# Kernel tuning notes

Measured on AMD Instinct MI355X. Metric: run time of the kernel, lower is better.

## Reference

```python
import jax, jax.numpy as jnp
import numpy as np

B, T, D, H, O, E = 4, 2048, 1024, 2048, 1024, 8
EPS = 1e-12  # torch F.normalize p=1 eps


def setup_inputs() -> dict:
    key = jax.random.key(0)
    ks = jax.random.split(key, 8)
    s = lambda *dims: 1.0 / np.sqrt(dims[0])
    return {
        "x": jax.random.normal(ks[0], (B, T, D), dtype=jnp.float32),
        "num_experts_chosen": 2,
        "W_gate": jax.random.normal(ks[1], (D, E), dtype=jnp.float32) * s(D),
        "b_gate": jnp.zeros((E,), dtype=jnp.float32),
        "W1": jax.random.normal(ks[2], (E, D, H), dtype=jnp.float32) * s(D),
        "b1": jnp.zeros((E, H), dtype=jnp.float32),
        "W2": jax.random.normal(ks[3], (E, H, O), dtype=jnp.float32) * s(H),
        "b2": jnp.zeros((E, O), dtype=jnp.float32),
    }


def reference(x, num_experts_chosen, W_gate, b_gate, W1, b1, W2, b2):
    # Router: softmax over experts -> [b, t, E]
    gating = jax.nn.softmax(jnp.einsum("btd,de->bte", x, W_gate) + b_gate, axis=-1)

    # Top-k mask (scatter of ones at top-k indices), then L1 renormalize
    _, topk_idx = jax.lax.top_k(gating, num_experts_chosen)  # [b, t, k]
    mask = jax.nn.one_hot(topk_idx, E, dtype=gating.dtype).sum(axis=-2)  # [b, t, E]
    g = gating * mask
    g = g / jnp.maximum(jnp.sum(jnp.abs(g), axis=-1, keepdims=True), EPS)

    # Dense compute of ALL experts (faithful to original), eval-mode dropout = identity
    h = jax.nn.relu(jnp.einsum("btd,edh->bteh", x, W1) + b1)  # [b, t, E, H]
    eo = jnp.einsum("bteh,eho->bteo", h, W2) + b2              # [b, t, E, O]

    # Weighted combine over experts
    return jnp.einsum("bte,bteo->bto", g, eo)
```

## Files before the change

kernel.cpp:

```cpp
#include <hip/hip_runtime.h>
#include <hip/hip_bf16.h>

typedef unsigned short u16;
typedef __attribute__((ext_vector_type(8))) short short8;
typedef __attribute__((ext_vector_type(4))) float floatx4;

#define NB 4
#define NT 2048
#define ND 1024
#define NH 2048
#define NO 1024
#define NE 8
#define NTOK (NB * NT)

#define BM2 256
#define BN2 256
#define BKT 64
#define TBUF 16384

__device__ __forceinline__ u16 f2bf(float f) {
  __hip_bfloat16 h = __float2bfloat16(f);
  return *reinterpret_cast<u16*>(&h);
}

__device__ __forceinline__ float bf2f(unsigned u) {
  return __uint_as_float(u << 16);
}

__device__ __forceinline__ void async16(const u16* g, u16* l) {
  __builtin_amdgcn_global_load_lds(
      (const __attribute__((address_space(1))) void*)g,
      (__attribute__((address_space(3))) void*)l, 16, 0, 0);
}

__global__ __launch_bounds__(256) void transpose_cvt(
    const float* __restrict__ in, u16* __restrict__ out, int R, int C) {
  __shared__ float tile[64][65];
  int e = blockIdx.z;
  in  += (size_t)e * R * C;
  out += (size_t)e * R * C;
  int c0 = blockIdx.x * 64, r0 = blockIdx.y * 64;
  int t = threadIdx.x;
#pragma unroll
  for (int i = 0; i < 4; ++i) {
    int idx = t + i * 256;
    int r = idx >> 4, cq = idx & 15;
    float4 v = *(const float4*)&in[(size_t)(r0 + r) * C + c0 + cq * 4];
    tile[r][cq * 4 + 0] = v.x; tile[r][cq * 4 + 1] = v.y;
    tile[r][cq * 4 + 2] = v.z; tile[r][cq * 4 + 3] = v.w;
  }
  __syncthreads();
#pragma unroll
  for (int i = 0; i < 4; ++i) {
    int idx = t + i * 256;
    int c = idx >> 4, rq = idx & 15;
    uint2 p;
    p.x = (unsigned)f2bf(tile[rq * 4 + 0][c]) | ((unsigned)f2bf(tile[rq * 4 + 1][c]) << 16);
    p.y = (unsigned)f2bf(tile[rq * 4 + 2][c]) | ((unsigned)f2bf(tile[rq * 4 + 3][c]) << 16);
    *(uint2*)&out[(size_t)(c0 + c) * R + r0 + rq * 4] = p;
  }
}

__global__ __launch_bounds__(256) void router_kernel(
    const float* __restrict__ x, const float* __restrict__ Wg,
    const float* __restrict__ bg, u16* __restrict__ xbf,
    int* __restrict__ counts, int* __restrict__ entries,
    float* __restrict__ wts) {
  __shared__ int   se0[32], se1[32];
  __shared__ float sw0[32], sw1[32];
  int t = threadIdx.x;
  int tl = t >> 3;
  int l8 = t & 7;
  int tok = blockIdx.x * 32 + tl;

  const float* xrow = x + (size_t)tok * ND;
  u16* xbrow = xbf + (size_t)tok * ND;
  float acc[8] = {};
#pragma unroll 4
  for (int i = 0; i < 32; ++i) {
    int d0 = l8 * 4 + i * 32;
    float4 xv = *(const float4*)&xrow[d0];
    uint2 p;
    p.x = (unsigned)f2bf(xv.x) | ((unsigned)f2bf(xv.y) << 16);
    p.y = (unsigned)f2bf(xv.z) | ((unsigned)f2bf(xv.w) << 16);
    *(uint2*)&xbrow[d0] = p;
    const float* wr = Wg + (size_t)d0 * NE;
#pragma unroll
    for (int j = 0; j < 4; ++j) {
      float xs = (j == 0) ? xv.x : (j == 1) ? xv.y : (j == 2) ? xv.z : xv.w;
      float4 w0 = *(const float4*)&wr[j * NE];
      float4 w1 = *(const float4*)&wr[j * NE + 4];
      acc[0] += xs * w0.x; acc[1] += xs * w0.y;
      acc[2] += xs * w0.z; acc[3] += xs * w0.w;
      acc[4] += xs * w1.x; acc[5] += xs * w1.y;
      acc[6] += xs * w1.z; acc[7] += xs * w1.w;
    }
  }
#pragma unroll
  for (int off = 4; off; off >>= 1)
#pragma unroll
    for (int k = 0; k < 8; ++k) acc[k] += __shfl_down(acc[k], off, 8);

  if (l8 == 0) {
    float best = -1e30f, second = -1e30f;
    int e0 = 0, e1 = 0;
#pragma unroll
    for (int i = 0; i < NE; ++i) {
      float L = acc[i] + bg[i];
      if (L > best) { second = best; e1 = e0; best = L; e0 = i; }
      else if (L > second) { second = L; e1 = i; }
    }
    float p1 = __expf(second - best);
    float inv = 1.f / (1.f + p1);
    se0[tl] = e0; se1[tl] = e1;
    sw0[tl] = inv; sw1[tl] = p1 * inv;
  }
  __syncthreads();

  if (t < NE) {
    int e = t;
    int c = 0;
#pragma unroll
    for (int k = 0; k < 32; ++k) c += (se0[k] == e) + (se1[k] == e);
    int pos = atomicAdd(&counts[e * 32], c);
    int base = blockIdx.x * 32;
    for (int k = 0; k < 32; ++k) {
      if (se0[k] == e) { entries[e * NTOK + pos] = (base + k) * 2;     wts[e * NTOK + pos] = sw0[k]; ++pos; }
      if (se1[k] == e) { entries[e * NTOK + pos] = (base + k) * 2 + 1; wts[e * NTOK + pos] = sw1[k]; ++pos; }
    }
  }
}

template<int KD, int NTILES, bool G2>
__global__ __launch_bounds__(512, 2) void gemm_moe(
    const u16* __restrict__ A, const u16* __restrict__ Bw,
    const float* __restrict__ bias, const int* __restrict__ counts,
    const int* __restrict__ entries, const float* __restrict__ wts,
    u16* __restrict__ out) {
  constexpr int LDO = NTILES * 256;
  constexpr int NI  = KD / 128;

  int b = blockIdx.x;
  int e = b & 7;
  int r = b >> 3;
  int m0 = (r / NTILES) * BM2;
  int n0 = (r % NTILES) * BN2;
  int cnt = counts[e * 32];
  if (m0 >= cnt) return;
  int rem = cnt - m0; if (rem > BM2) rem = BM2;

  __shared__ __align__(16) u16 As[2 * TBUF];
  __shared__ __align__(16) u16 Bs[2 * TBUF];
  __shared__ int   ent_s[BM2];
  __shared__ float w_s[BM2];

  int t = threadIdx.x;
  if (t < BM2) {
    int src = (t < rem) ? (e * NTOK + m0 + t) : (e * NTOK);
    ent_s[t] = entries[src];
    if constexpr (G2) w_s[t] = wts[src];
  }
  __syncthreads();

  int lane = t & 63, wv = t >> 6;
  int wr = wv >> 2, wc = wv & 3;

  int srow = lane >> 3;
  int sc   = ((lane & 7) ^ (srow & 7)) * 8;
  const u16* aS[2][2];
  const u16* bS[2][2];
#pragma unroll
  for (int h = 0; h < 2; ++h)
#pragma unroll
    for (int d = 0; d < 2; ++d) {
      int rowl = h * 128 + wv * 16 + d * 8 + srow;
      int ent = ent_s[rowl];
      size_t ra = G2 ? (size_t)ent : (size_t)(ent >> 1);
      aS[h][d] = A + ra * KD + sc;
      bS[h][d] = Bw + (size_t)e * LDO * KD + (size_t)(n0 + rowl) * KD + sc;
    }

#define STAGE_A(buf, half, ko) do { int _k = (ko); if (_k >= KD) _k = 0;    \
    async16(aS[half][0] + _k, As + (buf)*TBUF + (half)*8192 + wv*1024);      \
    async16(aS[half][1] + _k, As + (buf)*TBUF + (half)*8192 + wv*1024 + 512);\
  } while (0)
#define STAGE_B(buf, half, ko) do { int _k = (ko); if (_k >= KD) _k = 0;    \
    async16(bS[half][0] + _k, Bs + (buf)*TBUF + (half)*8192 + wv*1024);      \
    async16(bS[half][1] + _k, Bs + (buf)*TBUF + (half)*8192 + wv*1024 + 512);\
  } while (0)

  int rA = lane & 15, q = lane >> 4;
  int aRow = (wr * 64 + rA) * 64;
  int bRow = (wc * 32 + rA) * 64;
  int ch0 = ((q) ^ (rA & 7)) * 8;
  int ch1 = ((4 + q) ^ (rA & 7)) * 8;

  short8 a[2][4];
  short8 bb[2][2][2];
  floatx4 acc[2][2][4][2] = {};

#define LDA(mh, buf) do {                                                   \
    const u16* _p = As + (buf)*TBUF + (mh)*8192 + aRow;                      \
    _Pragma("unroll") for (int f = 0; f < 4; ++f) {                          \
      a[0][f] = *(const short8*)(_p + f*1024 + ch0);                         \
      a[1][f] = *(const short8*)(_p + f*1024 + ch1); } } while (0)
#define LDB(nh, buf) do {                                                   \
    const u16* _p = Bs + (buf)*TBUF + (nh)*8192 + bRow;                      \
    _Pragma("unroll") for (int nf = 0; nf < 2; ++nf) {                       \
      bb[nh][0][nf] = *(const short8*)(_p + nf*1024 + ch0);                  \
      bb[nh][1][nf] = *(const short8*)(_p + nf*1024 + ch1); } } while (0)
#define MM(mh, nh)                                                           \
    __builtin_amdgcn_s_setprio(1);                                           \
    _Pragma("unroll") for (int kk = 0; kk < 2; ++kk)                         \
    _Pragma("unroll") for (int f = 0; f < 4; ++f)                            \
    _Pragma("unroll") for (int nf = 0; nf < 2; ++nf)                         \
      acc[mh][nh][f][nf] = __builtin_amdgcn_mfma_f32_16x16x32_bf16(          \
          a[kk][f], bb[nh][kk][nf], acc[mh][nh][f][nf], 0, 0, 0);            \
    __builtin_amdgcn_s_setprio(0);
#define SCH __builtin_amdgcn_sched_barrier(0)
#define BAR __builtin_amdgcn_s_barrier()
#define LGK asm volatile("s_waitcnt lgkmcnt(0)")
#define VM6 asm volatile("s_waitcnt vmcnt(6)")

  STAGE_A(0, 0, 0);  STAGE_B(0, 0, 0);  STAGE_A(0, 1, 0);  STAGE_B(0, 1, 0);
  STAGE_A(1, 0, 64); STAGE_B(1, 0, 64); STAGE_A(1, 1, 64);
  SCH; VM6; SCH; BAR;

  for (int it = 0; it < NI; ++it) {
    int kb = it * 128;
    LDA(0, 0); LDB(0, 0);
    STAGE_B(1, 1, 64 + kb);
    SCH; BAR; LGK; SCH;
    MM(0, 0);
    SCH; BAR;
    LDB(1, 0);
    STAGE_A(0, 0, 128 + kb);
    SCH; BAR; LGK; SCH;
    MM(0, 1);
    SCH; BAR;
    LDA(1, 0);
    STAGE_B(0, 0, 128 + kb);
    SCH; BAR; LGK; SCH;
    MM(1, 0);
    SCH; BAR;
    STAGE_A(0, 1, 128 + kb);
    SCH; BAR; LGK; SCH;
    MM(1, 1);
    SCH; VM6; SCH; BAR;
    LDA(0, 1); LDB(0, 1);
    STAGE_B(0, 1, 128 + kb);
    SCH; BAR; LGK; SCH;
    MM(0, 0);
    SCH; BAR;
    LDB(1, 1);
    STAGE_A(1, 0, 192 + kb);
    SCH; BAR; LGK; SCH;
    MM(0, 1);
    SCH; BAR;
    LDA(1, 1);
    STAGE_B(1, 0, 192 + kb);
    SCH; BAR; LGK; SCH;
    MM(1, 0);
    SCH; BAR;
    STAGE_A(1, 1, 192 + kb);
    SCH; BAR; LGK; SCH;
    MM(1, 1);
    SCH; VM6; SCH; BAR;
  }
  SCH;
  asm volatile("s_waitcnt vmcnt(0)");
  SCH;

  float bcol[2][2];
#pragma unroll
  for (int nh = 0; nh < 2; ++nh)
#pragma unroll
    for (int nf = 0; nf < 2; ++nf)
      bcol[nh][nf] = bias[e * LDO + n0 + wc * 32 + nh * 128 + nf * 16 + rA];

#pragma unroll
  for (int mh = 0; mh < 2; ++mh)
#pragma unroll
    for (int f = 0; f < 4; ++f)
#pragma unroll
      for (int rr = 0; rr < 4; ++rr) {
        int lm = wr * 64 + mh * 128 + f * 16 + q * 4 + rr;
        if (lm >= rem) continue;
        int ent = ent_s[lm];
        float wgt = 1.f;
        if constexpr (G2) wgt = w_s[lm];
        u16* dst = out + (size_t)ent * LDO + n0;
#pragma unroll
        for (int nh = 0; nh < 2; ++nh)
#pragma unroll
          for (int nf = 0; nf < 2; ++nf) {
            int col = wc * 32 + nh * 128 + nf * 16 + rA;
            float v = acc[mh][nh][f][nf][rr] + bcol[nh][nf];
            if constexpr (G2) v *= wgt; else v = fmaxf(v, 0.f);
            dst[col] = f2bf(v);
          }
      }
#undef STAGE_A
#undef STAGE_B
#undef LDA
#undef LDB
#undef MM
#undef SCH
#undef BAR
#undef LGK
#undef VM6
}

__global__ __launch_bounds__(256) void combine_kernel(
    const u16* __restrict__ eo, float* __restrict__ out) {
  size_t idx = (size_t)blockIdx.x * 256 + threadIdx.x;
  size_t tok = idx >> 8;
  int oq = (int)(idx & 255) * 4;
  const u16* p0 = eo + (tok * 2) * NO + oq;
  const u16* p1 = p0 + NO;
  uint2 ua = *(const uint2*)p0;
  uint2 ub = *(const uint2*)p1;
  float4 o;
  o.x = bf2f(ua.x & 0xffff) + bf2f(ub.x & 0xffff);
  o.y = bf2f(ua.x >> 16)    + bf2f(ub.x >> 16);
  o.z = bf2f(ua.y & 0xffff) + bf2f(ub.y & 0xffff);
  o.w = bf2f(ua.y >> 16)    + bf2f(ub.y >> 16);
  *(float4*)&out[tok * NO + oq] = o;
}

extern "C" void kernel_launch(void* const* d_in, const int* in_sizes, int n_in,
                              void* d_out, int out_size, void* d_ws, size_t ws_size,
                              hipStream_t stream) {
  (void)in_sizes; (void)n_in; (void)out_size; (void)ws_size;
  const float* x  = (const float*)d_in[0];
  const float* Wg = (const float*)d_in[2];
  const float* bg = (const float*)d_in[3];
  const float* W1 = (const float*)d_in[4];
  const float* b1 = (const float*)d_in[5];
  const float* W2 = (const float*)d_in[6];
  const float* b2 = (const float*)d_in[7];
  float* out = (float*)d_out;

  char* ws = (char*)d_ws;
  size_t off = 0;
  int*   counts  = (int*)(ws + off);   off += NE * 32 * 4;
  int*   entries = (int*)(ws + off);   off += (size_t)NE * NTOK * 4;
  float* wts     = (float*)(ws + off); off += (size_t)NE * NTOK * 4;
  u16*   xbf     = (u16*)(ws + off);   off += (size_t)NTOK * ND * 2;
  u16*   w1t     = (u16*)(ws + off);   off += (size_t)NE * NH * ND * 2;
  u16*   w2t     = (u16*)(ws + off);   off += (size_t)NE * NO * NH * 2;
  u16*   hbuf    = (u16*)(ws + off);   off += (size_t)NTOK * 2 * NH * 2;
  u16*   eo      = w1t;

  hipMemsetAsync(counts, 0, NE * 32 * 4, stream);

  transpose_cvt<<<dim3(NH / 64, ND / 64, NE), 256, 0, stream>>>(W1, w1t, ND, NH);
  transpose_cvt<<<dim3(NO / 64, NH / 64, NE), 256, 0, stream>>>(W2, w2t, NH, NO);
  router_kernel<<<NTOK / 32, 256, 0, stream>>>(x, Wg, bg, xbf, counts, entries, wts);
  gemm_moe<ND, 8, false><<<NE * (NTOK / BM2) * 8, 512, 0, stream>>>(
      xbf, w1t, b1, counts, entries, wts, hbuf);
  gemm_moe<NH, 4, true ><<<NE * (NTOK / BM2) * 4, 512, 0, stream>>>(
      hbuf, w2t, b2, counts, entries, wts, eo);
  combine_kernel<<<(NTOK * NO / 4) / 256, 256, 0, stream>>>(eo, out);
}
```

Measured before the change: 482.8 us.

## Add triple-buffered async-LDS gather GEMM for first expert layer

Adds a new gemm_flow kernel that uses a three-stage LDS ring with BK=32 slices, issuing global_load_lds for tile k+2 while running MFMAs on tile k, with one barrier per iteration, a vmcnt wait, and raised wave priority around the MFMA block. It replaces gemm_moe for the first (x·W1, ReLU) GEMM only. The goal is to hide global-load latency behind compute with a simpler steady-state pipeline. In exchange it uses 96 KB of LDS per block, which may limit occupancy, and it takes more loop iterations with smaller K slices.

```diff
diff --git a/kernel.cpp b/kernel.cpp
--- a/kernel.cpp
+++ b/kernel.cpp
@@ -15,7 +15,6 @@
 
 #define BM2 256
 #define BN2 256
-#define BKT 64
 #define TBUF 16384
 
 __device__ __forceinline__ u16 f2bf(float f) {
@@ -127,6 +126,125 @@
     for (int k = 0; k < 32; ++k) {
       if (se0[k] == e) { entries[e * NTOK + pos] = (base + k) * 2;     wts[e * NTOK + pos] = sw0[k]; ++pos; }
       if (se1[k] == e) { entries[e * NTOK + pos] = (base + k) * 2 + 1; wts[e * NTOK + pos] = sw1[k]; ++pos; }
+    }
+  }
+}
+
+template<int KD, int NTILES, bool G2>
+__global__ __launch_bounds__(512, 2) void gemm_flow(
+    const u16* __restrict__ A, const u16* __restrict__ Bw,
+    const float* __restrict__ bias, const int* __restrict__ counts,
+    const int* __restrict__ entries, const float* __restrict__ wts,
+    u16* __restrict__ out) {
+  constexpr int LDO = NTILES * 256;
+  constexpr int NKT = KD / 32;
+
+  int b = blockIdx.x;
+  int e = b & 7;
+  int r = b >> 3;
+  int m0 = (r / NTILES) * BM2;
+  int n0 = (r % NTILES) * BN2;
+  int cnt = counts[e * 32];
+  if (m0 >= cnt) return;
+  int rem = cnt - m0; if (rem > BM2) rem = BM2;
+
+  __shared__ __align__(16) u16 As[3 * 8192];
+  __shared__ __align__(16) u16 Bs[3 * 8192];
+  __shared__ int   ent_s[BM2];
+  __shared__ float w_s[BM2];
+
+  int t = threadIdx.x;
+  if (t < BM2) {
+    int src = (t < rem) ? (e * NTOK + m0 + t) : (e * NTOK);
+    ent_s[t] = entries[src];
+    if constexpr (G2) w_s[t] = wts[src];
+  }
+  __syncthreads();
+
+  int lane = t & 63, wv = t >> 6;
+  int wr = wv >> 2, wc = wv & 3;
+
+  int rl0 = wv * 16 + (lane >> 2);
+  int rl1 = rl0 + 128;
+  int pg = ((lane & 3) ^ ((rl0 >> 1) & 3)) * 8;
+  int eA0 = ent_s[rl0], eA1 = ent_s[rl1];
+  size_t ra0 = G2 ? (size_t)eA0 : (size_t)(eA0 >> 1);
+  size_t ra1 = G2 ? (size_t)eA1 : (size_t)(eA1 >> 1);
+  const u16* pA0 = A + ra0 * KD + pg;
+  const u16* pA1 = A + ra1 * KD + pg;
+  const u16* Bbase = Bw + (size_t)e * LDO * KD + (size_t)n0 * KD;
+  const u16* pB0 = Bbase + (size_t)rl0 * KD + pg;
+  const u16* pB1 = Bbase + (size_t)rl1 * KD + pg;
+  int d0 = wv * 512, d1 = 4096 + wv * 512;
+
+  int rA = lane & 15, q = lane >> 4;
+  int pOff = rA * 32 + ((q ^ ((rA >> 1) & 3)) * 8);
+  int aOff = wr * 4096 + pOff;
+  int bOff = wc * 2048 + pOff;
+
+  floatx4 acc[8][4] = {};
+
+  async16(pA0, As + d0);        async16(pA1, As + d1);
+  async16(pB0, Bs + d0);        async16(pB1, Bs + d1);
+  async16(pA0 + 32, As + 8192 + d0); async16(pA1 + 32, As + 8192 + d1);
+  async16(pB0 + 32, Bs + 8192 + d0); async16(pB1 + 32, Bs + 8192 + d1);
+  __builtin_amdgcn_sched_barrier(0);
+  asm volatile("s_waitcnt vmcnt(4)");
+  __builtin_amdgcn_sched_barrier(0);
+  __builtin_amdgcn_s_barrier();
+
+  int rb = 0, sb = 2;
+  for (int kt = 0; kt < NKT; ++kt) {
+    const u16* Ab = As + rb * 8192;
+    const u16* Bb = Bs + rb * 8192;
+    u16* Ad = As + sb * 8192;
+    u16* Bd = Bs + sb * 8192;
+    int k2 = (kt + 2 < NKT) ? (kt + 2) * 32 : 0;
+    short8 a[8], bv[4];
+#pragma unroll
+    for (int i = 0; i < 4; ++i) a[i] = *(const short8*)(Ab + aOff + i * 512);
+#pragma unroll
+    for (int g = 0; g < 4; ++g) bv[g] = *(const short8*)(Bb + bOff + g * 512);
+#pragma unroll
+    for (int i = 4; i < 8; ++i) a[i] = *(const short8*)(Ab + aOff + i * 512);
+    async16(pA0 + k2, Ad + d0);
+    async16(pA1 + k2, Ad + d1);
+    async16(pB0 + k2, Bd + d0);
+    async16(pB1 + k2, Bd + d1);
+    __builtin_amdgcn_s_setprio(1);
+#pragma unroll
+    for (int i = 0; i < 8; ++i)
+#pragma unroll
+      for (int g = 0; g < 4; ++g)
+        acc[i][g] = __builtin_amdgcn_mfma_f32_16x16x32_bf16(a[i], bv[g], acc[i][g], 0, 0, 0);
+    __builtin_amdgcn_s_setprio(0);
+    rb = (rb == 2) ? 0 : rb + 1;
+    sb = (sb == 2) ? 0 : sb + 1;
+    __builtin_amdgcn_sched_barrier(0);
+    asm volatile("s_waitcnt vmcnt(4)");
+    __builtin_amdgcn_sched_barrier(0);
+    __builtin_amdgcn_s_barrier();
+  }
+  asm volatile("s_waitcnt vmcnt(0)");
+
+  const float* brow = bias + (size_t)e * LDO + n0 + wc * 64;
+#pragma unroll
+  for (int f = 0; f < 8; ++f) {
+#pragma unroll
+    for (int rr = 0; rr < 4; ++rr) {
+      int lm = wr * 128 + f * 16 + q * 4 + rr;
+      if (lm >= rem) continue;
+      int ent = ent_s[lm];
+      float wgt = 1.f;
+      if constexpr (G2) wgt = w_s[lm];
+      u16* dst = out + (size_t)ent * LDO + n0 + wc * 64;
+#pragma unroll
+      for (int g = 0; g < 4; ++g) {
+        int col = g * 16 + rA;
+        float v = acc[f][g][rr] + brow[col];
+        if constexpr (G2) v *= wgt; else v = fmaxf(v, 0.f);
+        dst[col] = f2bf(v);
+      }
     }
   }
 }
@@ -357,7 +475,7 @@
   transpose_cvt<<<dim3(NH / 64, ND / 64, NE), 256, 0, stream>>>(W1, w1t, ND, NH);
   transpose_cvt<<<dim3(NO / 64, NH / 64, NE), 256, 0, stream>>>(W2, w2t, NH, NO);
   router_kernel<<<NTOK / 32, 256, 0, stream>>>(x, Wg, bg, xbf, counts, entries, wts);
-  gemm_moe<ND, 8, false><<<NE * (NTOK / BM2) * 8, 512, 0, stream>>>(
+  gemm_flow<ND, 8, false><<<NE * (NTOK / BM2) * 8, 512, 0, stream>>>(
       xbf, w1t, b1, counts, entries, wts, hbuf);
   gemm_moe<NH, 4, true ><<<NE * (NTOK / BM2) * 4, 512, 0, stream>>>(
       hbuf, w2t, b2, counts, entries, wts, eo);
```

After: 481.5 us. Within noise of the previous version (-0.3%).
